# Performance work log

Measured on AMD Instinct MI355X. Metric: run time of the kernel, lower is better.

Reference implementation:

```python
import jax, jax.numpy as jnp
import numpy as np

N = 50000
IN_F = 128
OUT_F = 128
NRELA = 128
E1 = 400000
E2 = 100000
ALPHA = 0.2   # LeakyReLU slope
D = 0.85      # PageRank damping
EPS = 1e-12


def setup_inputs() -> dict:
    key = jax.random.key(0)
    ks = jax.random.split(key, 8)
    return {
        "input": jax.random.normal(ks[0], (N, IN_F), dtype=jnp.float32),
        "edge": jax.random.randint(ks[1], (2, E1), 0, N, dtype=jnp.int64),
        "edge_embed": jax.random.normal(ks[2], (E1, NRELA), dtype=jnp.float32),
        "edge_list_nhop": jax.random.randint(ks[3], (2, E2), 0, N, dtype=jnp.int64),
        "edge_embed_nhop": jax.random.normal(ks[4], (E2, NRELA), dtype=jnp.float32),
        "entity_rank": jax.random.uniform(ks[5], (N,), dtype=jnp.float32),
        "a": 0.05 * jax.random.normal(ks[6], (OUT_F, 2 * IN_F + NRELA), dtype=jnp.float32),
        "a_2": 0.05 * jax.random.normal(ks[7], (1, OUT_F), dtype=jnp.float32),
    }


def reference(input, edge, edge_embed, edge_list_nhop, edge_embed_nhop, entity_rank, a, a_2):
    n = input.shape[0]
    # concat n-hop edges (len(edge_list_nhop) != 0 path in the original)
    e = jnp.concatenate([edge, edge_list_nhop], axis=1)          # [2, E]
    emb = jnp.concatenate([edge_embed, edge_embed_nhop], axis=0) # [E, nrela]
    src, dst = e[0], e[1]

    # edge MLP: edge_h = [x_src | x_dst | rel]  -> a @ edge_h^T, leakyrelu
    edge_h = jnp.concatenate([input[src], input[dst], emb], axis=1)   # [E, 2*in+nrela]
    edge_m = jax.nn.leaky_relu(edge_h @ a.T, ALPHA)                   # [E, out]
    powers = -jax.nn.leaky_relu(edge_m @ a_2[0], ALPHA)               # [E]
    edge_e = jnp.exp(powers)                                          # [E]

    # softmax-like normalization over incoming edges of each target node
    a_rowsum = jax.ops.segment_sum(edge_e, dst, num_segments=n)       # [N]
    a_rowsum = jnp.where(a_rowsum == 0.0, EPS, a_rowsum)
    rel_att = edge_e / a_rowsum[dst]                                  # [E]

    # PageRank-style rank update
    e_rowsum = jax.ops.segment_sum(rel_att, src, num_segments=n)      # [N] (out-sum)
    e_rowsum = jnp.where(e_rowsum == 0.0, EPS, e_rowsum)
    val = rel_att * entity_rank[src] / e_rowsum[src]                  # [E]
    e_colsum = jax.ops.segment_sum(val, dst, num_segments=n)          # [N]
    new_rank = 1.0 - D + D * e_colsum                                 # [N]

    # rank-weighted attention propagation of edge features
    edge_prop = (rel_att * new_rank[src])[:, None] * edge_m           # [E, out]
    h_prime = jax.ops.segment_sum(edge_prop, dst, num_segments=n)     # [N, out]

    return jax.nn.elu(h_prime), new_rank
```

## Files before the change

### kernel.cpp

```cpp
#include <hip/hip_runtime.h>
#include <math.h>

#define N_NODES 50000
#define E1N 400000
#define E2N 100000
#define E_TOT 500000
#define ALPHAC 0.2f
#define DAMP 0.85f
#define EPSC 1e-12f

typedef __bf16 bf16_t;
typedef __bf16 bf16x4 __attribute__((ext_vector_type(4)));
typedef __bf16 bf16x8 __attribute__((ext_vector_type(8)));
typedef _Float16 f16_t;
typedef _Float16 f16x4 __attribute__((ext_vector_type(4)));
typedef float f32x4 __attribute__((ext_vector_type(4)));
typedef float f32x16 __attribute__((ext_vector_type(16)));

__device__ __forceinline__ float lrelu(float x) { return x > 0.f ? x : ALPHAC * x; }

__global__ __launch_bounds__(256) void k_pack12(const float* __restrict__ a,
                                                bf16_t* __restrict__ bp) {
  int i = blockIdx.x * 256 + threadIdx.x;
  if (i >= 32768) return;
  int j = i & 7;
  int l = (i >> 3) & 63;
  int nt = (i >> 9) & 7;
  int ks = i >> 12;
  int c = nt * 32 + (l & 31);
  int o = (c < 128) ? c : c - 128;
  int koff = (c < 128) ? 0 : 128;
  int k = ks * 16 + ((l >> 5) << 3) + j;
  bp[i] = (bf16_t)a[o * 384 + koff + k];
}

__global__ __launch_bounds__(256) void k_pack3(const float* __restrict__ a,
                                               bf16_t* __restrict__ bp) {
  int i = blockIdx.x * 256 + threadIdx.x;
  if (i >= 16384) return;
  int j = i & 7;
  int l = (i >> 3) & 63;
  int nt = (i >> 9) & 3;
  int ks = i >> 11;
  int o = nt * 32 + (l & 31);
  int k = ks * 16 + ((l >> 5) << 3) + j;
  bp[i] = (bf16_t)a[o * 384 + 256 + k];
}

__global__ __launch_bounds__(256) void k_pack3c(const float* __restrict__ a,
                                                bf16_t* __restrict__ bp) {
  int i = blockIdx.x * 256 + threadIdx.x;
  if (i >= 16384) return;
  int j = i & 7;
  int l = (i >> 3) & 63;
  int nt = (i >> 9) & 7;
  int ks = i >> 12;
  int o = nt * 16 + (l & 15);
  int k = ks * 32 + ((l >> 4) << 3) + j;
  bp[i] = (bf16_t)a[o * 384 + 256 + k];
}

__global__ __launch_bounds__(256) void k_edges(const int* __restrict__ edge,
                                               const int* __restrict__ nhop,
                                               int* __restrict__ sidx,
                                               int* __restrict__ didx, int stride,
                                               int* __restrict__ cnt) {
  int e = blockIdx.x * 256 + threadIdx.x;
  if (e >= E_TOT) return;
  int s, d;
  if (e < E1N) {
    s = edge[(size_t)e * stride];
    d = edge[(size_t)(E1N + e) * stride];
  } else {
    int t = e - E1N;
    s = nhop[(size_t)t * stride];
    d = nhop[(size_t)(E2N + t) * stride];
  }
  sidx[e] = s;
  didx[e] = d;
  if (cnt) atomicAdd(&cnt[d], 1);
}

__global__ __launch_bounds__(256) void k_scan(const int* __restrict__ cnt,
                                              int* __restrict__ csr_start,
                                              int* __restrict__ cursor) {
  __shared__ int ls[256];
  __shared__ int lofs[256];
  int t = threadIdx.x;
  int lo = t * 196, hi = lo + 196;
  if (hi > N_NODES) hi = N_NODES;
  int s = 0;
  for (int i = lo; i < hi; ++i) s += cnt[i];
  ls[t] = s;
  __syncthreads();
  if (t == 0) {
    int run = 0;
    for (int i = 0; i < 256; ++i) { lofs[i] = run; run += ls[i]; }
  }
  __syncthreads();
  int run = lofs[t];
  for (int i = lo; i < hi; ++i) {
    csr_start[i] = run;
    cursor[i] = run;
    run += cnt[i];
  }
}

__global__ __launch_bounds__(256) void k_pos(const int* __restrict__ didx,
                                             int* __restrict__ cursor,
                                             int* __restrict__ eid) {
  int e = blockIdx.x * 256 + threadIdx.x;
  if (e >= E_TOT) return;
  int pos = atomicAdd(&cursor[didx[e]], 1);
  eid[pos] = e;
}

__global__ __launch_bounds__(256) void k_uv(const float* __restrict__ input,
                                            const bf16_t* __restrict__ bp12,
                                            bf16_t* __restrict__ uv) {
  const int tid = threadIdx.x, lane = tid & 63, wv = tid >> 6;
  const int n0 = blockIdx.x * 128 + wv * 32;
  const int m = lane & 31, hi2 = lane >> 5;
  int n = n0 + m;
  if (n >= N_NODES) n = 0;
  const float* ar = input + (size_t)n * 128 + hi2 * 8;
  const bf16x8* bp = (const bf16x8*)bp12;

  f32x16 acc[8];
#pragma unroll
  for (int nt = 0; nt < 8; ++nt)
#pragma unroll
    for (int r = 0; r < 16; ++r) acc[nt][r] = 0.f;

#pragma unroll
  for (int ks = 0; ks < 8; ++ks) {
    float4 u0 = *(const float4*)(ar + ks * 16);
    float4 u1 = *(const float4*)(ar + ks * 16 + 4);
    bf16x8 af = {(bf16_t)u0.x, (bf16_t)u0.y, (bf16_t)u0.z, (bf16_t)u0.w,
                 (bf16_t)u1.x, (bf16_t)u1.y, (bf16_t)u1.z, (bf16_t)u1.w};
#pragma unroll
    for (int nt = 0; nt < 8; ++nt)
      acc[nt] = __builtin_amdgcn_mfma_f32_32x32x16_bf16(af, bp[(ks * 8 + nt) * 64 + lane],
                                                        acc[nt], 0, 0, 0);
  }
#pragma unroll
  for (int nt = 0; nt < 8; ++nt)
#pragma unroll
    for (int r = 0; r < 16; ++r) {
      int row = (r & 3) + ((r >> 2) << 3) + (hi2 << 2);
      int node = n0 + row;
      if (node < N_NODES) uv[(size_t)node * 256 + nt * 32 + m] = (bf16_t)acc[nt][r];
    }
}

__global__ __launch_bounds__(256) void k_passA3(
    const float* __restrict__ eemb, const float* __restrict__ eembn,
    const bf16_t* __restrict__ uv, const int* __restrict__ sidx,
    const int* __restrict__ didx, const bf16_t* __restrict__ bp3c,
    const float* __restrict__ a2, float* __restrict__ edge_e,
    float* __restrict__ a_rowsum, bf16_t* __restrict__ P) {
  __shared__ __align__(16) char s_raw[16384];
  const int tid = threadIdx.x;
  const long long e0 = (long long)blockIdx.x * 64;

#pragma unroll
  for (int s = 0; s < 8; ++s) {
    int idx = s * 1024 + tid * 4;
    int row = idx >> 7, col = idx & 127;
    long long e = e0 + row;
    float4 u = make_float4(0.f, 0.f, 0.f, 0.f);
    if (e < E_TOT) {
      const float* src = (e < E1N) ? eemb + (size_t)e * 128
                                   : eembn + (size_t)(e - E1N) * 128;
      u = *(const float4*)(src + col);
    }
    bf16x4 b = {(bf16_t)u.x, (bf16_t)u.y, (bf16_t)u.z, (bf16_t)u.w};
    *(bf16x4*)(s_raw + row * 256 + ((col * 2) ^ ((row & 7) << 4))) = b;
  }
  __syncthreads();

  const int lane = tid & 63, wv = tid >> 6;
  const int cc = lane & 15, kg = lane >> 4;
  const int arow = wv * 16 + cc;
  const int swz = (arow & 7) << 4;
  const bf16x8* bpc = (const bf16x8*)bp3c;

  f32x4 acc[8];
#pragma unroll
  for (int nt = 0; nt < 8; ++nt) acc[nt] = (f32x4){0.f, 0.f, 0.f, 0.f};

#pragma unroll
  for (int ks = 0; ks < 4; ++ks) {
    bf16x8 af = *(const bf16x8*)(s_raw + arow * 256 + ((ks * 64 + kg * 16) ^ swz));
#pragma unroll
    for (int nt = 0; nt < 8; ++nt)
      acc[nt] = __builtin_amdgcn_mfma_f32_16x16x32_bf16(
          af, bpc[(ks * 8 + nt) * 64 + lane], acc[nt], 0, 0, 0);
  }
  __syncthreads();

#pragma unroll
  for (int nt = 0; nt < 8; ++nt)
#pragma unroll
    for (int r = 0; r < 4; ++r) {
      int row = wv * 16 + kg * 4 + r;
      int cb = (nt * 16 + cc) * 2;
      *(f16_t*)(s_raw + row * 256 + (cb ^ ((row & 7) << 4))) = (f16_t)acc[nt][r];
    }
  __syncthreads();

  {
    const int g = tid >> 5;
    const int ml = tid & 31;
    const int cl = ml * 4;
    const float4 a2v = *(const float4*)(a2 + cl);
    int sarr[8], darr[8];
#pragma unroll
    for (int i = 0; i < 8; ++i) {
      long long e = e0 + i * 8 + g;
      sarr[i] = 0;
      darr[i] = 0;
      if (e < E_TOT) {
        sarr[i] = sidx[e];
        darr[i] = didx[e];
      }
    }
#pragma unroll
    for (int i = 0; i < 8; ++i) {
      int row = i * 8 + g;
      long long e = e0 + row;
      if (e >= E_TOT) break;
      bf16x4 uu = *(const bf16x4*)(uv + (size_t)sarr[i] * 256 + cl);
      bf16x4 vv = *(const bf16x4*)(uv + (size_t)darr[i] * 256 + 128 + cl);
      f16x4 cc4 = *(const f16x4*)(s_raw + row * 256 + ((cl * 2) ^ ((row & 7) << 4)));
      float p0 = lrelu((float)cc4[0] + (float)uu[0] + (float)vv[0]);
      float p1 = lrelu((float)cc4[1] + (float)uu[1] + (float)vv[1]);
      float p2 = lrelu((float)cc4[2] + (float)uu[2] + (float)vv[2]);
      float p3 = lrelu((float)cc4[3] + (float)uu[3] + (float)vv[3]);
      bf16x4 po = {(bf16_t)p0, (bf16_t)p1, (bf16_t)p2, (bf16_t)p3};
      *(bf16x4*)(P + (size_t)e * 128 + cl) = po;
      float sac = p0 * a2v.x + p1 * a2v.y + p2 * a2v.z + p3 * a2v.w;
#pragma unroll
      for (int off = 1; off < 32; off <<= 1) sac += __shfl_xor(sac, off, 64);
      if (ml == 0) {
        float ev = expf(-lrelu(sac));
        edge_e[e] = ev;
        atomicAdd(&a_rowsum[darr[i]], ev);
      }
    }
  }
}

__global__ __launch_bounds__(256) void k_hprime(const bf16_t* __restrict__ P,
                                                const int* __restrict__ eid,
                                                const int* __restrict__ csr_start,
                                                const int* __restrict__ cnt,
                                                const float* __restrict__ rel_att,
                                                const int* __restrict__ sidx,
                                                const float* __restrict__ new_rank,
                                                float* __restrict__ out) {
  int g = (blockIdx.x << 3) | (threadIdx.x >> 5);
  if (g >= N_NODES) return;
  int m = threadIdx.x & 31;
  int start = csr_start[g], deg = cnt[g];
  float a0 = 0.f, a1 = 0.f, a2v = 0.f, a3v = 0.f;
  for (int i = 0; i < deg; ++i) {
    int e = eid[start + i];
    float we = rel_att[e] * new_rank[sidx[e]];
    bf16x4 p = *(const bf16x4*)(P + (size_t)e * 128 + m * 4);
    a0 += we * (float)p[0];
    a1 += we * (float)p[1];
    a2v += we * (float)p[2];
    a3v += we * (float)p[3];
  }
  float4 r;
  r.x = a0 > 0.f ? a0 : expm1f(a0);
  r.y = a1 > 0.f ? a1 : expm1f(a1);
  r.z = a2v > 0.f ? a2v : expm1f(a2v);
  r.w = a3v > 0.f ? a3v : expm1f(a3v);
  *(float4*)(out + (size_t)g * 128 + m * 4) = r;
}

template <bool ACCUM>
__global__ __launch_bounds__(256, 3) void k_pass(
    const float* __restrict__ eemb, const float* __restrict__ eembn,
    const bf16_t* __restrict__ uv, const int* __restrict__ sidx,
    const int* __restrict__ didx, const bf16_t* __restrict__ bp3,
    const float* __restrict__ a2, float* __restrict__ edge_e,
    float* __restrict__ a_rowsum, const float* __restrict__ rel_att,
    const float* __restrict__ new_rank, float* __restrict__ hout) {
  __shared__ bf16_t s_sum[128][136];
  const int tid = threadIdx.x;
  const long long e0 = (long long)blockIdx.x * 128;
  {
    const int g = tid >> 5;
    const int cl = (tid & 31) * 4;
#pragma unroll
    for (int i = 0; i < 16; ++i) {
      int el = i * 8 + g;
      long long e = e0 + el;
      float sx = 0.f, sy = 0.f, sz = 0.f, sw = 0.f;
      if (e < E_TOT) {
        int s = sidx[e], d = didx[e];
        bf16x4 u = *(const bf16x4*)(uv + (size_t)s * 256 + cl);
        bf16x4 v = *(const bf16x4*)(uv + (size_t)d * 256 + 128 + cl);
        sx = (float)u[0] + (float)v[0];
        sy = (float)u[1] + (float)v[1];
        sz = (float)u[2] + (float)v[2];
        sw = (float)u[3] + (float)v[3];
      }
      bf16x4 o = {(bf16_t)sx, (bf16_t)sy, (bf16_t)sz, (bf16_t)sw};
      *(bf16x4*)&s_sum[el][cl] = o;
    }
  }
  __syncthreads();

  const int lane = tid & 63;
  const int wv = tid >> 6;
  const long long e0w = e0 + wv * 32;
  if (e0w >= E_TOT) return;
  const int m = lane & 31, hi2 = lane >> 5;
  const long long e = e0w + m;
  const float* b2 = (e < E1N) ? (eemb + (size_t)e * 128)
                              : (eembn + (size_t)(e - E1N) * 128);
  const float* ar = b2 + hi2 * 8;

  const bf16x8* bp = (const bf16x8*)bp3;
  f32x16 acc[4];
#pragma unroll
  for (int nt = 0; nt < 4; ++nt)
#pragma unroll
    for (int r = 0; r < 16; ++r) acc[nt][r] = 0.f;

  auto loadA = [&](int ks) -> bf16x8 {
    float4 u0 = *(const float4*)(ar + ks * 16);
    float4 u1 = *(const float4*)(ar + ks * 16 + 4);
    bf16x8 rr = {(bf16_t)u0.x, (bf16_t)u0.y, (bf16_t)u0.z, (bf16_t)u0.w,
                 (bf16_t)u1.x, (bf16_t)u1.y, (bf16_t)u1.z, (bf16_t)u1.w};
    return rr;
  };

  bf16x8 a_cur = loadA(0);
  bf16x8 bb[4], bn[4];
#pragma unroll
  for (int nt = 0; nt < 4; ++nt) bb[nt] = bp[nt * 64 + lane];

#pragma unroll
  for (int ks = 0; ks < 8; ++ks) {
    bf16x8 a_nxt;
    if (ks < 7) {
      a_nxt = loadA(ks + 1);
#pragma unroll
      for (int nt = 0; nt < 4; ++nt) bn[nt] = bp[((ks + 1) * 4 + nt) * 64 + lane];
    }
#pragma unroll
    for (int nt = 0; nt < 4; ++nt)
      acc[nt] = __builtin_amdgcn_mfma_f32_32x32x16_bf16(a_cur, bb[nt], acc[nt], 0, 0, 0);
    a_cur = a_nxt;
#pragma unroll
    for (int nt = 0; nt < 4; ++nt) bb[nt] = bn[nt];
  }

  if (!ACCUM) {
    float sac[16];
#pragma unroll
    for (int r = 0; r < 16; ++r) sac[r] = 0.f;
#pragma unroll
    for (int nt = 0; nt < 4; ++nt) {
      float a2v = a2[nt * 32 + m];
      int o = nt * 32 + m;
#pragma unroll
      for (int r = 0; r < 16; ++r) {
        int row = (r & 3) + ((r >> 2) << 3) + (hi2 << 2);
        float c = acc[nt][r] + (float)s_sum[wv * 32 + row][o];
        sac[r] += lrelu(c) * a2v;
      }
    }
#pragma unroll
    for (int off = 1; off < 32; off <<= 1) {
#pragma unroll
      for (int r = 0; r < 16; ++r) sac[r] += __shfl_xor(sac[r], off, 64);
    }
    if (m == 0) {
#pragma unroll
      for (int r = 0; r < 16; ++r) {
        int row = (r & 3) + ((r >> 2) << 3) + (hi2 << 2);
        long long ee_i = e0w + row;
        float ev = expf(-lrelu(sac[r]));
        edge_e[ee_i] = ev;
        atomicAdd(&a_rowsum[didx[ee_i]], ev);
      }
    }
  } else {
    float w_m = rel_att[e] * new_rank[sidx[e]];
    int d = didx[e];
    float wr[16];
    int dr[16];
#pragma unroll
    for (int r = 0; r < 16; ++r) {
      int row = (r & 3) + ((r >> 2) << 3) + (hi2 << 2);
      wr[r] = __shfl(w_m, row, 64);
      dr[r] = __shfl(d, row, 64);
    }
#pragma unroll
    for (int nt = 0; nt < 4; ++nt) {
      int o = nt * 32 + m;
#pragma unroll
      for (int r = 0; r < 16; ++r) {
        int row = (r & 3) + ((r >> 2) << 3) + (hi2 << 2);
        float c = acc[nt][r] + (float)s_sum[wv * 32 + row][o];
        atomicAdd(&hout[(size_t)dr[r] * 128 + o], lrelu(c) * wr[r]);
      }
    }
  }
}

__global__ __launch_bounds__(256) void k_relatt(const float* __restrict__ edge_e,
                                                const int* __restrict__ didx,
                                                const int* __restrict__ sidx,
                                                const float* __restrict__ a_rowsum,
                                                float* __restrict__ rel_att,
                                                float* __restrict__ e_rowsum) {
  int e = blockIdx.x * 256 + threadIdx.x;
  if (e >= E_TOT) return;
  float rs = a_rowsum[didx[e]];
  rs = (rs == 0.f) ? EPSC : rs;
  float r = edge_e[e] / rs;
  rel_att[e] = r;
  atomicAdd(&e_rowsum[sidx[e]], r);
}

__global__ __launch_bounds__(256) void k_val(const float* __restrict__ rel_att,
                                             const int* __restrict__ sidx,
                                             const int* __restrict__ didx,
                                             const float* __restrict__ rank,
                                             const float* __restrict__ e_rowsum,
                                             float* __restrict__ e_colsum) {
  int e = blockIdx.x * 256 + threadIdx.x;
  if (e >= E_TOT) return;
  int s = sidx[e];
  float er = e_rowsum[s];
  er = (er == 0.f) ? EPSC : er;
  float val = rel_att[e] * rank[s] / er;
  atomicAdd(&e_colsum[didx[e]], val);
}

__global__ __launch_bounds__(256) void k_rank(const float* __restrict__ e_colsum,
                                              float* __restrict__ new_rank,
                                              float* __restrict__ out_tail) {
  int n = blockIdx.x * 256 + threadIdx.x;
  if (n >= N_NODES) return;
  float nr = 1.f - DAMP + DAMP * e_colsum[n];
  new_rank[n] = nr;
  out_tail[n] = nr;
}

__global__ __launch_bounds__(256) void k_elu(float* __restrict__ h) {
  int i = blockIdx.x * 256 + threadIdx.x;
  if (i < N_NODES * 128) {
    float x = h[i];
    h[i] = x > 0.f ? x : expm1f(x);
  }
}

extern "C" void kernel_launch(void* const* d_in, const int* in_sizes, int n_in,
                              void* d_out, int out_size, void* d_ws, size_t ws_size,
                              hipStream_t stream) {
  const float* input = (const float*)d_in[0];
  const int* edge = (const int*)d_in[1];
  const float* eemb = (const float*)d_in[2];
  const int* enh = (const int*)d_in[3];
  const float* eembn = (const float*)d_in[4];
  const float* rank = (const float*)d_in[5];
  const float* a = (const float*)d_in[6];
  const float* a2 = (const float*)d_in[7];
  float* out = (float*)d_out;

  int estride = (in_sizes[1] == 2 * E1N) ? 1 : 2;

  char* ws = (char*)d_ws;
  bf16_t* bp12 = (bf16_t*)(ws);
  bf16_t* bp3 = (bf16_t*)(ws + 65536);
  bf16_t* bp3c = (bf16_t*)(ws + 98304);
  bf16_t* uv = (bf16_t*)(ws + 131072);
  int* sidx = (int*)(ws + 25731072);
  int* didx = (int*)(ws + 27731072);
  float* edge_e = (float*)(ws + 29731072);
  float* rel_att = (float*)(ws + 31731072);
  int* eid = (int*)(ws + 33731072);
  int* csr_start = (int*)(ws + 35731072);
  int* cursor = (int*)(ws + 35931072);
  int* cnt = (int*)(ws + 36131072);
  float* a_rowsum = (float*)(ws + 36331072);
  float* e_rowsum = (float*)(ws + 36531072);
  float* e_colsum = (float*)(ws + 36731072);
  float* new_rank = (float*)(ws + 36931072);
  bf16_t* P = (bf16_t*)(ws + 37131264);

  const bool big = ws_size >= 165131264ULL;

  const int NB = (E_TOT + 127) / 128;
  const int NB3 = (E_TOT + 63) / 64;
  const int EB = (E_TOT + 255) / 256;

  if (big) {
    hipMemsetAsync(cnt, 0, 4 * 200000, stream);

    k_pack12<<<128, 256, 0, stream>>>(a, bp12);
    k_pack3c<<<64, 256, 0, stream>>>(a, bp3c);
    k_edges<<<EB, 256, 0, stream>>>(edge, enh, sidx, didx, estride, cnt);
    k_scan<<<1, 256, 0, stream>>>(cnt, csr_start, cursor);
    k_pos<<<EB, 256, 0, stream>>>(didx, cursor, eid);
    k_uv<<<(N_NODES + 127) / 128, 256, 0, stream>>>(input, bp12, uv);

    k_passA3<<<NB3, 256, 0, stream>>>(eemb, eembn, uv, sidx, didx, bp3c, a2,
                                      edge_e, a_rowsum, P);
    k_relatt<<<EB, 256, 0, stream>>>(edge_e, didx, sidx, a_rowsum, rel_att, e_rowsum);
    k_val<<<EB, 256, 0, stream>>>(rel_att, sidx, didx, rank, e_rowsum, e_colsum);
    k_rank<<<(N_NODES + 255) / 256, 256, 0, stream>>>(e_colsum, new_rank,
                                                      out + (size_t)N_NODES * 128);
    k_hprime<<<(N_NODES + 7) / 8, 256, 0, stream>>>(P, eid, csr_start, cnt, rel_att,
                                                    sidx, new_rank, out);
  } else {
    hipMemsetAsync(cnt, 0, 4 * 200000, stream);
    hipMemsetAsync(out, 0, (size_t)N_NODES * 128 * 4, stream);

    k_pack12<<<128, 256, 0, stream>>>(a, bp12);
    k_pack3<<<64, 256, 0, stream>>>(a, bp3);
    k_edges<<<EB, 256, 0, stream>>>(edge, enh, sidx, didx, estride, nullptr);
    k_uv<<<(N_NODES + 127) / 128, 256, 0, stream>>>(input, bp12, uv);

    k_pass<false><<<NB, 256, 0, stream>>>(eemb, eembn, uv, sidx, didx, bp3, a2,
                                          edge_e, a_rowsum, nullptr, nullptr, nullptr);
    k_relatt<<<EB, 256, 0, stream>>>(edge_e, didx, sidx, a_rowsum, rel_att, e_rowsum);
    k_val<<<EB, 256, 0, stream>>>(rel_att, sidx, didx, rank, e_rowsum, e_colsum);
    k_rank<<<(N_NODES + 255) / 256, 256, 0, stream>>>(e_colsum, new_rank,
                                                      out + (size_t)N_NODES * 128);
    k_pass<true><<<NB, 256, 0, stream>>>(eemb, eembn, uv, sidx, didx, bp3, a2,
                                         nullptr, nullptr, rel_att, new_rank, out);
    k_elu<<<(N_NODES * 128 + 255) / 256, 256, 0, stream>>>(out);
  }
}
```

Baseline: 744.0 us.

## Store edge data in dst-sorted CSR order and prefetch in edge MLP kernel

Edges are now written into destination-sorted positions: P, edge_e and sidx/didx are stored at their CSR slot, so the h_prime gather reads contiguous rows instead of chasing an eid indirection. The count pass is split out of the index-copy kernel. The edge MLP kernel loads indices, the weight tile (staged into LDS) and uv rows up front so these loads overlap. The uv GEMM is split into two half-width blocks for more parallelism, and h_prime software-prefetches the next edge. In exchange, P and edge_e writes become scattered, and rel_att is computed in place over edge_e.

```diff
diff --git a/kernel.cpp b/kernel.cpp
--- a/kernel.cpp
+++ b/kernel.cpp
@@ -60,11 +60,20 @@
   bp[i] = (bf16_t)a[o * 384 + 256 + k];
 }
 
+__global__ __launch_bounds__(256) void k_cnt(const int* __restrict__ edge,
+                                             const int* __restrict__ nhop,
+                                             int stride, int* __restrict__ cnt) {
+  int e = blockIdx.x * 256 + threadIdx.x;
+  if (e >= E_TOT) return;
+  int d = (e < E1N) ? edge[(size_t)(E1N + e) * stride]
+                    : nhop[(size_t)(E2N + (e - E1N)) * stride];
+  atomicAdd(&cnt[d], 1);
+}
+
 __global__ __launch_bounds__(256) void k_edges(const int* __restrict__ edge,
                                                const int* __restrict__ nhop,
                                                int* __restrict__ sidx,
-                                               int* __restrict__ didx, int stride,
-                                               int* __restrict__ cnt) {
+                                               int* __restrict__ didx, int stride) {
   int e = blockIdx.x * 256 + threadIdx.x;
   if (e >= E_TOT) return;
   int s, d;
@@ -78,7 +87,6 @@
   }
   sidx[e] = s;
   didx[e] = d;
-  if (cnt) atomicAdd(&cnt[d], 1);
 }
 
 __global__ __launch_bounds__(256) void k_scan(const int* __restrict__ cnt,
@@ -106,29 +114,45 @@
   }
 }
 
-__global__ __launch_bounds__(256) void k_pos(const int* __restrict__ didx,
-                                             int* __restrict__ cursor,
-                                             int* __restrict__ eid) {
+__global__ __launch_bounds__(256) void k_pos2(const int* __restrict__ edge,
+                                              const int* __restrict__ nhop,
+                                              int stride, int* __restrict__ cursor,
+                                              int* __restrict__ epos,
+                                              int* __restrict__ sidx_s,
+                                              int* __restrict__ didx_s) {
   int e = blockIdx.x * 256 + threadIdx.x;
   if (e >= E_TOT) return;
-  int pos = atomicAdd(&cursor[didx[e]], 1);
-  eid[pos] = e;
-}
-
-__global__ __launch_bounds__(256) void k_uv(const float* __restrict__ input,
-                                            const bf16_t* __restrict__ bp12,
-                                            bf16_t* __restrict__ uv) {
+  int s, d;
+  if (e < E1N) {
+    s = edge[(size_t)e * stride];
+    d = edge[(size_t)(E1N + e) * stride];
+  } else {
+    int t = e - E1N;
+    s = nhop[(size_t)t * stride];
+    d = nhop[(size_t)(E2N + t) * stride];
+  }
+  int pos = atomicAdd(&cursor[d], 1);
+  epos[e] = pos;
+  sidx_s[pos] = s;
+  didx_s[pos] = d;
+}
+
+__global__ __launch_bounds__(256) void k_uv2(const float* __restrict__ input,
+                                             const bf16_t* __restrict__ bp12,
+                                             bf16_t* __restrict__ uv) {
   const int tid = threadIdx.x, lane = tid & 63, wv = tid >> 6;
-  const int n0 = blockIdx.x * 128 + wv * 32;
+  const int blk = blockIdx.x >> 1, half = blockIdx.x & 1;
+  const int ntoff = half * 4;
+  const int n0 = blk * 128 + wv * 32;
   const int m = lane & 31, hi2 = lane >> 5;
   int n = n0 + m;
   if (n >= N_NODES) n = 0;
   const float* ar = input + (size_t)n * 128 + hi2 * 8;
   const bf16x8* bp = (const bf16x8*)bp12;
 
-  f32x16 acc[8];
-#pragma unroll
-  for (int nt = 0; nt < 8; ++nt)
+  f32x16 acc[4];
+#pragma unroll
+  for (int nt = 0; nt < 4; ++nt)
 #pragma unroll
     for (int r = 0; r < 16; ++r) acc[nt][r] = 0.f;
 
@@ -139,51 +163,98 @@
     bf16x8 af = {(bf16_t)u0.x, (bf16_t)u0.y, (bf16_t)u0.z, (bf16_t)u0.w,
                  (bf16_t)u1.x, (bf16_t)u1.y, (bf16_t)u1.z, (bf16_t)u1.w};
 #pragma unroll
-    for (int nt = 0; nt < 8; ++nt)
-      acc[nt] = __builtin_amdgcn_mfma_f32_32x32x16_bf16(af, bp[(ks * 8 + nt) * 64 + lane],
-                                                        acc[nt], 0, 0, 0);
-  }
-#pragma unroll
-  for (int nt = 0; nt < 8; ++nt)
+    for (int nt = 0; nt < 4; ++nt)
+      acc[nt] = __builtin_amdgcn_mfma_f32_32x32x16_bf16(
+          af, bp[(ks * 8 + ntoff + nt) * 64 + lane], acc[nt], 0, 0, 0);
+  }
+#pragma unroll
+  for (int nt = 0; nt < 4; ++nt)
 #pragma unroll
     for (int r = 0; r < 16; ++r) {
       int row = (r & 3) + ((r >> 2) << 3) + (hi2 << 2);
       int node = n0 + row;
-      if (node < N_NODES) uv[(size_t)node * 256 + nt * 32 + m] = (bf16_t)acc[nt][r];
-    }
-}
-
-__global__ __launch_bounds__(256) void k_passA3(
+      if (node < N_NODES)
+        uv[(size_t)node * 256 + (ntoff + nt) * 32 + m] = (bf16_t)acc[nt][r];
+    }
+}
+
+__global__ __launch_bounds__(256) void k_passA4(
     const float* __restrict__ eemb, const float* __restrict__ eembn,
-    const bf16_t* __restrict__ uv, const int* __restrict__ sidx,
-    const int* __restrict__ didx, const bf16_t* __restrict__ bp3c,
-    const float* __restrict__ a2, float* __restrict__ edge_e,
-    float* __restrict__ a_rowsum, bf16_t* __restrict__ P) {
-  __shared__ __align__(16) char s_raw[16384];
+    const bf16_t* __restrict__ uv, const int* __restrict__ edge,
+    const int* __restrict__ nhop, int stride, const int* __restrict__ epos,
+    const bf16_t* __restrict__ bp3c, const float* __restrict__ a2,
+    float* __restrict__ edge_e_s, float* __restrict__ a_rowsum,
+    bf16_t* __restrict__ P) {
+  __shared__ __align__(16) char sA[16384];
+  __shared__ __align__(16) char sB[32768];
   const int tid = threadIdx.x;
   const long long e0 = (long long)blockIdx.x * 64;
-
+  const int lane = tid & 63;
+
+  const int strow = tid >> 5;
+  const int stcol = (tid & 31) * 4;
+  float4 rg[8];
 #pragma unroll
   for (int s = 0; s < 8; ++s) {
-    int idx = s * 1024 + tid * 4;
-    int row = idx >> 7, col = idx & 127;
+    int row = s * 8 + strow;
     long long e = e0 + row;
-    float4 u = make_float4(0.f, 0.f, 0.f, 0.f);
+    rg[s] = make_float4(0.f, 0.f, 0.f, 0.f);
     if (e < E_TOT) {
       const float* src = (e < E1N) ? eemb + (size_t)e * 128
                                    : eembn + (size_t)(e - E1N) * 128;
-      u = *(const float4*)(src + col);
-    }
-    bf16x4 b = {(bf16_t)u.x, (bf16_t)u.y, (bf16_t)u.z, (bf16_t)u.w};
-    *(bf16x4*)(s_raw + row * 256 + ((col * 2) ^ ((row & 7) << 4))) = b;
+      rg[s] = *(const float4*)(src + stcol);
+    }
+  }
+  int4 rb[8];
+  {
+    const int4* bsrc = (const int4*)bp3c;
+#pragma unroll
+    for (int i = 0; i < 8; ++i) rb[i] = bsrc[i * 256 + tid];
+  }
+  const int g = tid >> 5;
+  const int ml = tid & 31;
+  int sarr[8], darr[8], parr[8];
+#pragma unroll
+  for (int i = 0; i < 8; ++i) {
+    long long e = e0 + i * 8 + g;
+    sarr[i] = 0; darr[i] = 0; parr[i] = 0;
+    if (e < E_TOT) {
+      if (e < E1N) {
+        sarr[i] = edge[(size_t)e * stride];
+        darr[i] = edge[(size_t)(E1N + e) * stride];
+      } else {
+        long long t = e - E1N;
+        sarr[i] = nhop[(size_t)t * stride];
+        darr[i] = nhop[(size_t)(E2N + t) * stride];
+      }
+      parr[i] = epos[e];
+    }
+  }
+#pragma unroll
+  for (int s = 0; s < 8; ++s) {
+    int row = s * 8 + strow;
+    bf16x4 b = {(bf16_t)rg[s].x, (bf16_t)rg[s].y, (bf16_t)rg[s].z, (bf16_t)rg[s].w};
+    *(bf16x4*)(sA + row * 256 + ((stcol * 2) ^ ((row & 7) << 4))) = b;
+  }
+  {
+    int4* bdst = (int4*)sB;
+#pragma unroll
+    for (int i = 0; i < 8; ++i) bdst[i * 256 + tid] = rb[i];
+  }
+  const int cl = ml * 4;
+  bf16x4 uu[8], vv[8];
+#pragma unroll
+  for (int i = 0; i < 8; ++i) {
+    uu[i] = *(const bf16x4*)(uv + (size_t)sarr[i] * 256 + cl);
+    vv[i] = *(const bf16x4*)(uv + (size_t)darr[i] * 256 + 128 + cl);
   }
   __syncthreads();
 
-  const int lane = tid & 63, wv = tid >> 6;
+  const int wv = tid >> 6;
   const int cc = lane & 15, kg = lane >> 4;
   const int arow = wv * 16 + cc;
   const int swz = (arow & 7) << 4;
-  const bf16x8* bpc = (const bf16x8*)bp3c;
+  const bf16x8* sBv = (const bf16x8*)sB;
 
   f32x4 acc[8];
 #pragma unroll
@@ -191,11 +262,11 @@
 
 #pragma unroll
   for (int ks = 0; ks < 4; ++ks) {
-    bf16x8 af = *(const bf16x8*)(s_raw + arow * 256 + ((ks * 64 + kg * 16) ^ swz));
+    bf16x8 af = *(const bf16x8*)(sA + arow * 256 + ((ks * 64 + kg * 16) ^ swz));
 #pragma unroll
     for (int nt = 0; nt < 8; ++nt)
       acc[nt] = __builtin_amdgcn_mfma_f32_16x16x32_bf16(
-          af, bpc[(ks * 8 + nt) * 64 + lane], acc[nt], 0, 0, 0);
+          af, sBv[(ks * 8 + nt) * 64 + lane], acc[nt], 0, 0, 0);
   }
   __syncthreads();
 
@@ -205,80 +276,70 @@
     for (int r = 0; r < 4; ++r) {
       int row = wv * 16 + kg * 4 + r;
       int cb = (nt * 16 + cc) * 2;
-      *(f16_t*)(s_raw + row * 256 + (cb ^ ((row & 7) << 4))) = (f16_t)acc[nt][r];
+      *(f16_t*)(sA + row * 256 + (cb ^ ((row & 7) << 4))) = (f16_t)acc[nt][r];
     }
   __syncthreads();
 
   {
-    const int g = tid >> 5;
-    const int ml = tid & 31;
-    const int cl = ml * 4;
     const float4 a2v = *(const float4*)(a2 + cl);
-    int sarr[8], darr[8];
-#pragma unroll
-    for (int i = 0; i < 8; ++i) {
-      long long e = e0 + i * 8 + g;
-      sarr[i] = 0;
-      darr[i] = 0;
-      if (e < E_TOT) {
-        sarr[i] = sidx[e];
-        darr[i] = didx[e];
-      }
-    }
 #pragma unroll
     for (int i = 0; i < 8; ++i) {
       int row = i * 8 + g;
       long long e = e0 + row;
-      if (e >= E_TOT) break;
-      bf16x4 uu = *(const bf16x4*)(uv + (size_t)sarr[i] * 256 + cl);
-      bf16x4 vv = *(const bf16x4*)(uv + (size_t)darr[i] * 256 + 128 + cl);
-      f16x4 cc4 = *(const f16x4*)(s_raw + row * 256 + ((cl * 2) ^ ((row & 7) << 4)));
-      float p0 = lrelu((float)cc4[0] + (float)uu[0] + (float)vv[0]);
-      float p1 = lrelu((float)cc4[1] + (float)uu[1] + (float)vv[1]);
-      float p2 = lrelu((float)cc4[2] + (float)uu[2] + (float)vv[2]);
-      float p3 = lrelu((float)cc4[3] + (float)uu[3] + (float)vv[3]);
-      bf16x4 po = {(bf16_t)p0, (bf16_t)p1, (bf16_t)p2, (bf16_t)p3};
-      *(bf16x4*)(P + (size_t)e * 128 + cl) = po;
-      float sac = p0 * a2v.x + p1 * a2v.y + p2 * a2v.z + p3 * a2v.w;
-#pragma unroll
-      for (int off = 1; off < 32; off <<= 1) sac += __shfl_xor(sac, off, 64);
-      if (ml == 0) {
-        float ev = expf(-lrelu(sac));
-        edge_e[e] = ev;
-        atomicAdd(&a_rowsum[darr[i]], ev);
+      if (e < E_TOT) {
+        f16x4 cc4 = *(const f16x4*)(sA + row * 256 + ((cl * 2) ^ ((row & 7) << 4)));
+        float p0 = lrelu((float)cc4[0] + (float)uu[i][0] + (float)vv[i][0]);
+        float p1 = lrelu((float)cc4[1] + (float)uu[i][1] + (float)vv[i][1]);
+        float p2 = lrelu((float)cc4[2] + (float)uu[i][2] + (float)vv[i][2]);
+        float p3 = lrelu((float)cc4[3] + (float)uu[i][3] + (float)vv[i][3]);
+        bf16x4 po = {(bf16_t)p0, (bf16_t)p1, (bf16_t)p2, (bf16_t)p3};
+        *(bf16x4*)(P + (size_t)parr[i] * 128 + cl) = po;
+        float sac = p0 * a2v.x + p1 * a2v.y + p2 * a2v.z + p3 * a2v.w;
+#pragma unroll
+        for (int off = 1; off < 32; off <<= 1) sac += __shfl_xor(sac, off, 64);
+        if (ml == 0) {
+          float ev = expf(-lrelu(sac));
+          edge_e_s[parr[i]] = ev;
+          atomicAdd(&a_rowsum[darr[i]], ev);
+        }
       }
     }
   }
 }
 
-__global__ __launch_bounds__(256) void k_hprime(const bf16_t* __restrict__ P,
-                                                const int* __restrict__ eid,
-                                                const int* __restrict__ csr_start,
-                                                const int* __restrict__ cnt,
-                                                const float* __restrict__ rel_att,
-                                                const int* __restrict__ sidx,
-                                                const float* __restrict__ new_rank,
-                                                float* __restrict__ out) {
-  int g = (blockIdx.x << 3) | (threadIdx.x >> 5);
-  if (g >= N_NODES) return;
+__global__ __launch_bounds__(256) void k_hprime_s(
+    const bf16_t* __restrict__ P, const int* __restrict__ csr_start,
+    const int* __restrict__ cnt, const float* __restrict__ rel_att_s,
+    const int* __restrict__ sidx_s, const float* __restrict__ new_rank,
+    float* __restrict__ out) {
+  int gnode = (blockIdx.x << 3) | (threadIdx.x >> 5);
+  if (gnode >= N_NODES) return;
   int m = threadIdx.x & 31;
-  int start = csr_start[g], deg = cnt[g];
+  int start = csr_start[gnode], deg = cnt[gnode];
   float a0 = 0.f, a1 = 0.f, a2v = 0.f, a3v = 0.f;
-  for (int i = 0; i < deg; ++i) {
-    int e = eid[start + i];
-    float we = rel_att[e] * new_rank[sidx[e]];
-    bf16x4 p = *(const bf16x4*)(P + (size_t)e * 128 + m * 4);
-    a0 += we * (float)p[0];
-    a1 += we * (float)p[1];
-    a2v += we * (float)p[2];
-    a3v += we * (float)p[3];
+  if (deg > 0) {
+    float rel_c = rel_att_s[start];
+    float rk_c = new_rank[sidx_s[start]];
+    bf16x4 p_c = *(const bf16x4*)(P + (size_t)start * 128 + m * 4);
+    for (int i = 0; i < deg; ++i) {
+      int qn = start + ((i + 1 < deg) ? i + 1 : i);
+      float rel_n = rel_att_s[qn];
+      float rk_n = new_rank[sidx_s[qn]];
+      bf16x4 p_n = *(const bf16x4*)(P + (size_t)qn * 128 + m * 4);
+      float we = rel_c * rk_c;
+      a0 += we * (float)p_c[0];
+      a1 += we * (float)p_c[1];
+      a2v += we * (float)p_c[2];
+      a3v += we * (float)p_c[3];
+      rel_c = rel_n; rk_c = rk_n; p_c = p_n;
+    }
   }
   float4 r;
   r.x = a0 > 0.f ? a0 : expm1f(a0);
   r.y = a1 > 0.f ? a1 : expm1f(a1);
   r.z = a2v > 0.f ? a2v : expm1f(a2v);
   r.w = a3v > 0.f ? a3v : expm1f(a3v);
-  *(float4*)(out + (size_t)g * 128 + m * 4) = r;
+  *(float4*)(out + (size_t)gnode * 128 + m * 4) = r;
 }
 
 template <bool ACCUM>
@@ -480,64 +541,71 @@
 
   char* ws = (char*)d_ws;
   bf16_t* bp12 = (bf16_t*)(ws);
-  bf16_t* bp3 = (bf16_t*)(ws + 65536);
-  bf16_t* bp3c = (bf16_t*)(ws + 98304);
-  bf16_t* uv = (bf16_t*)(ws + 131072);
-  int* sidx = (int*)(ws + 25731072);
-  int* didx = (int*)(ws + 27731072);
-  float* edge_e = (float*)(ws + 29731072);
-  float* rel_att = (float*)(ws + 31731072);
-  int* eid = (int*)(ws + 33731072);
-  int* csr_start = (int*)(ws + 35731072);
-  int* cursor = (int*)(ws + 35931072);
-  int* cnt = (int*)(ws + 36131072);
-  float* a_rowsum = (float*)(ws + 36331072);
-  float* e_rowsum = (float*)(ws + 36531072);
-  float* e_colsum = (float*)(ws + 36731072);
-  float* new_rank = (float*)(ws + 36931072);
-  bf16_t* P = (bf16_t*)(ws + 37131264);
-
-  const bool big = ws_size >= 165131264ULL;
+  bf16_t* bp3s = (bf16_t*)(ws + 65536);
+  bf16_t* uv = (bf16_t*)(ws + 98304);
+  int* epos = (int*)(ws + 25698304);
+  int* sidx_s = (int*)(ws + 27698304);
+  int* didx_s = (int*)(ws + 29698304);
+  float* edge_e_s = (float*)(ws + 31698304);
+  int* csr_start = (int*)(ws + 33698304);
+  int* cursor = (int*)(ws + 33898304);
+  int* cnt = (int*)(ws + 34098304);
+  float* a_rowsum = (float*)(ws + 34298304);
+  float* e_rowsum = (float*)(ws + 34498304);
+  float* e_colsum = (float*)(ws + 34698304);
+  float* new_rank = (float*)(ws + 34898304);
+  bf16_t* P = (bf16_t*)(ws + 35098624);
+
+  const bool big = ws_size >= 163098624ULL;
 
   const int NB = (E_TOT + 127) / 128;
-  const int NB3 = (E_TOT + 63) / 64;
+  const int NB4 = (E_TOT + 63) / 64;
   const int EB = (E_TOT + 255) / 256;
+  const int UVB = 2 * ((N_NODES + 127) / 128);
 
   if (big) {
     hipMemsetAsync(cnt, 0, 4 * 200000, stream);
 
     k_pack12<<<128, 256, 0, stream>>>(a, bp12);
-    k_pack3c<<<64, 256, 0, stream>>>(a, bp3c);
-    k_edges<<<EB, 256, 0, stream>>>(edge, enh, sidx, didx, estride, cnt);
+    k_pack3c<<<64, 256, 0, stream>>>(a, bp3s);
+    k_cnt<<<EB, 256, 0, stream>>>(edge, enh, estride, cnt);
     k_scan<<<1, 256, 0, stream>>>(cnt, csr_start, cursor);
-    k_pos<<<EB, 256, 0, stream>>>(didx, cursor, eid);
-    k_uv<<<(N_NODES + 127) / 128, 256, 0, stream>>>(input, bp12, uv);
-
-    k_passA3<<<NB3, 256, 0, stream>>>(eemb, eembn, uv, sidx, didx, bp3c, a2,
-                                      edge_e, a_rowsum, P);
-    k_relatt<<<EB, 256, 0, stream>>>(edge_e, didx, sidx, a_rowsum, rel_att, e_rowsum);
-    k_val<<<EB, 256, 0, stream>>>(rel_att, sidx, didx, rank, e_rowsum, e_colsum);
+    k_pos2<<<EB, 256, 0, stream>>>(edge, enh, estride, cursor, epos, sidx_s, didx_s);
+    k_uv2<<<UVB, 256, 0, stream>>>(input, bp12, uv);
+
+    k_passA4<<<NB4, 256, 0, stream>>>(eemb, eembn, uv, edge, enh, estride, epos,
+                                      bp3s, a2, edge_e_s, a_rowsum, P);
+    k_relatt<<<EB, 256, 0, stream>>>(edge_e_s, didx_s, sidx_s, a_rowsum,
+                                     edge_e_s, e_rowsum);
+    k_val<<<EB, 256, 0, stream>>>(edge_e_s, sidx_s, didx_s, rank, e_rowsum, e_colsum);
     k_rank<<<(N_NODES + 255) / 256, 256, 0, stream>>>(e_colsum, new_rank,
                                                       out + (size_t)N_NODES * 128);
-    k_hprime<<<(N_NODES + 7) / 8, 256, 0, stream>>>(P, eid, csr_start, cnt, rel_att,
-                                                    sidx, new_rank, out);
+    k_hprime_s<<<(N_NODES + 7) / 8, 256, 0, stream>>>(P, csr_start, cnt, edge_e_s,
+                                                      sidx_s, new_rank, out);
   } else {
+    int* sidx_fb = epos;
+    int* didx_fb = sidx_s;
+    float* rel_fb = (float*)didx_s;
+    float* ee_fb = edge_e_s;
+
     hipMemsetAsync(cnt, 0, 4 * 200000, stream);
     hipMemsetAsync(out, 0, (size_t)N_NODES * 128 * 4, stream);
 
     k_pack12<<<128, 256, 0, stream>>>(a, bp12);
-    k_pack3<<<64, 256, 0, stream>>>(a, bp3);
-    k_edges<<<EB, 256, 0, stream>>>(edge, enh, sidx, didx, estride, nullptr);
-    k_uv<<<(N_NODES + 127) / 128, 256, 0, stream>>>(input, bp12, uv);
-
-    k_pass<false><<<NB, 256, 0, stream>>>(eemb, eembn, uv, sidx, didx, bp3, a2,
-                                          edge_e, a_rowsum, nullptr, nullptr, nullptr);
-    k_relatt<<<EB, 256, 0, stream>>>(edge_e, didx, sidx, a_rowsum, rel_att, e_rowsum);
-    k_val<<<EB, 256, 0, stream>>>(rel_att, sidx, didx, rank, e_rowsum, e_colsum);
+    k_pack3<<<64, 256, 0, stream>>>(a, bp3s);
+    k_edges<<<EB, 256, 0, stream>>>(edge, enh, sidx_fb, didx_fb, estride);
+    k_uv2<<<UVB, 256, 0, stream>>>(input, bp12, uv);
+
+    k_pass<false><<<NB, 256, 0, stream>>>(eemb, eembn, uv, sidx_fb, didx_fb, bp3s,
+                                          a2, ee_fb, a_rowsum, nullptr, nullptr,
+                                          nullptr);
+    k_relatt<<<EB, 256, 0, stream>>>(ee_fb, didx_fb, sidx_fb, a_rowsum, rel_fb,
+                                     e_rowsum);
+    k_val<<<EB, 256, 0, stream>>>(rel_fb, sidx_fb, didx_fb, rank, e_rowsum, e_colsum);
     k_rank<<<(N_NODES + 255) / 256, 256, 0, stream>>>(e_colsum, new_rank,
                                                       out + (size_t)N_NODES * 128);
-    k_pass<true><<<NB, 256, 0, stream>>>(eemb, eembn, uv, sidx, didx, bp3, a2,
-                                         nullptr, nullptr, rel_att, new_rank, out);
+    k_pass<true><<<NB, 256, 0, stream>>>(eemb, eembn, uv, sidx_fb, didx_fb, bp3s,
+                                         a2, nullptr, nullptr, rel_fb, new_rank, out);
     k_elu<<<(N_NODES * 128 + 255) / 256, 256, 0, stream>>>(out);
   }
 }
```

Result: no change. 753.4 us (+1.3%).
